# Optimization experiments

Measured on AMD Instinct MI355X. Metric: run time of the kernel, lower is better.

Reference implementation:

```python
import jax, jax.numpy as jnp
import numpy as np

EPS = 1e-5


def setup_inputs() -> dict:
    key = jax.random.key(0)
    ks = jax.random.split(key, 12)
    B, S, M, D, H, dh = 8, 512, 512, 1024, 16, 64
    T = S + M
    w_scale = 0.03  # keep attention logits in a sane range (mimics nn.Linear init scale)
    return {
        "x": jax.random.normal(ks[0], (B, S, D), jnp.float32),
        "mem": jax.random.normal(ks[1], (B, M, D), jnp.float32),
        "R": jax.random.normal(ks[2], (T, D), jnp.float32),
        "u": jax.random.normal(ks[3], (1, H, 1, dh), jnp.float32) * 0.1,
        "t": jax.random.normal(ks[4], (1, H, 1, dh), jnp.float32) * 0.1,
        "Wq": jax.random.normal(ks[5], (H * dh, D), jnp.float32) * w_scale,
        "Wk": jax.random.normal(ks[6], (H * dh, D), jnp.float32) * w_scale,
        "Wv": jax.random.normal(ks[7], (H * dh, D), jnp.float32) * w_scale,
        "Wr": jax.random.normal(ks[8], (H * dh, D), jnp.float32) * w_scale,
        "Wo": jax.random.normal(ks[9], (D, H * dh), jnp.float32) * w_scale,
        "gamma": jnp.ones((D,), jnp.float32),
        "beta": jnp.zeros((D,), jnp.float32),
    }


def reference(x, mem, R, u, t, Wq, Wk, Wv, Wr, Wo, gamma, beta):
    B, S, D = x.shape
    H, dh = u.shape[1], u.shape[3]
    h = jnp.concatenate([mem, x], axis=1)          # [B, T, D]
    T = h.shape[1]
    M = T - S

    q = (x @ Wq.T).reshape(B, S, H, dh).transpose(0, 2, 1, 3)   # [B,H,S,dh]
    k = (h @ Wk.T).reshape(B, T, H, dh).transpose(0, 2, 1, 3)   # [B,H,T,dh]
    v = (h @ Wv.T).reshape(B, T, H, dh).transpose(0, 2, 1, 3)   # [B,H,T,dh]
    r = (R[-T:] @ Wr.T).reshape(1, T, H, dh).transpose(0, 2, 1, 3)  # [1,H,T,dh]

    ac = jnp.einsum("bhid,bhjd->bhij", q + u, k)                # [B,H,S,T]
    bd = jnp.einsum("bhid,hjd->bhij", q + t, r[0])              # [B,H,S,T]

    # circulant shift: shifted[..., i, j] = bd[..., i, (j - i + S - 1) % T]
    idx = (jnp.arange(T)[None, :] - jnp.arange(S)[:, None] + S - 1) % T  # [S,T]
    bd = jnp.take_along_axis(bd, idx[None, None], axis=3)

    # causal mask with memory offset: keep j <= i + M (tril(mem_len)), then
    # exact-zero entries (the masked ones) become -inf, matching the original.
    mask = jnp.arange(T)[None, :] <= (jnp.arange(S)[:, None] + M)        # [S,T]
    score = jnp.where(mask[None, None], (ac + bd) / jnp.sqrt(jnp.float32(dh)), 0.0)
    score = jnp.where(score == 0, -jnp.inf, score)
    p = jax.nn.softmax(score, axis=-1)                                   # [B,H,S,T]

    att = jnp.einsum("bhij,bhjd->bhid", p, v).transpose(0, 2, 1, 3).reshape(B, S, H * dh)
    out = att @ Wo.T                                                      # dropout is identity (p=0/eval)

    y = out + x
    mu = jnp.mean(y, axis=-1, keepdims=True)
    var = jnp.var(y, axis=-1, keepdims=True)
    return (y - mu) / jnp.sqrt(var + EPS) * gamma + beta
```

## Files before the change

### kernel.cpp

```cpp
#include <hip/hip_runtime.h>
#include <math.h>

#define BB 8
#define SS 512
#define MM 512
#define TT 1024
#define DD 1024
#define HH 16
#define DH 64

typedef __attribute__((ext_vector_type(8))) short bf16x8;
typedef __attribute__((ext_vector_type(4))) float f32x4;

#define SCL2E 0.1803368801111f
#define DTHR 11.5f

__device__ __forceinline__ ushort f2bf(float f) {
  union { float f; unsigned u; } x; x.f = f;
  unsigned r = x.u + 0x7fffu + ((x.u >> 16) & 1u);
  return (ushort)(r >> 16);
}

__device__ __forceinline__ void stage16(void* lds, const void* g) {
  __builtin_amdgcn_global_load_lds((const __attribute__((address_space(1))) void*)g,
                                   (__attribute__((address_space(3))) void*)lds, 16, 0, 0);
}

template <int C>
__device__ __forceinline__ float dppf(float x) {
  return __builtin_bit_cast(float,
      __builtin_amdgcn_update_dpp(0, __builtin_bit_cast(int, x), C, 0xF, 0xF, true));
}
__device__ __forceinline__ float redmax16(float x) {
  x = fmaxf(x, dppf<0xB1>(x));
  x = fmaxf(x, dppf<0x4E>(x));
  x = fmaxf(x, dppf<0x141>(x));
  x = fmaxf(x, dppf<0x140>(x));
  return x;
}
__device__ __forceinline__ float redsum16(float x) {
  x += dppf<0xB1>(x);
  x += dppf<0x4E>(x);
  x += dppf<0x141>(x);
  x += dppf<0x140>(x);
  return x;
}
__device__ __forceinline__ float bperm_f(int byteaddr, float v) {
  return __builtin_bit_cast(float,
      __builtin_amdgcn_ds_bpermute(byteaddr, __builtin_bit_cast(int, v)));
}

__global__ __launch_bounds__(256) void cast_all(
    const float* __restrict__ mem, const float* __restrict__ x,
    const float* __restrict__ R, const float* __restrict__ Wq,
    const float* __restrict__ Wk, const float* __restrict__ Wv,
    const float* __restrict__ Wr, const float* __restrict__ Wo,
    ushort* __restrict__ hb, ushort* __restrict__ Rb, ushort* __restrict__ Wqb,
    ushort* __restrict__ Wkb, ushort* __restrict__ Wvb, ushort* __restrict__ Wrb,
    ushort* __restrict__ Wob) {
  const int M1 = 1 << 20;
  int i = (blockIdx.x * 256 + threadIdx.x) * 8;
  const float* src;
  ushort* dst;
  if (i < 4 * M1) {
    src = mem + i;
    dst = hb + (size_t)i + (size_t)(i >> 19) * 524288;
  } else if (i < 8 * M1) {
    int j = i - 4 * M1;
    src = x + j;
    dst = hb + (size_t)j + (size_t)(j >> 19) * 524288 + 524288;
  } else if (i < 9 * M1) {
    src = R + (i - 8 * M1);  dst = Rb + (i - 8 * M1);
  } else if (i < 10 * M1) {
    src = Wq + (i - 9 * M1); dst = Wqb + (i - 9 * M1);
  } else if (i < 11 * M1) {
    src = Wk + (i - 10 * M1); dst = Wkb + (i - 10 * M1);
  } else if (i < 12 * M1) {
    src = Wv + (i - 11 * M1); dst = Wvb + (i - 11 * M1);
  } else if (i < 13 * M1) {
    src = Wr + (i - 12 * M1); dst = Wrb + (i - 12 * M1);
  } else {
    src = Wo + (i - 13 * M1); dst = Wob + (i - 13 * M1);
  }
  float4 a = *(const float4*)(src);
  float4 c = *(const float4*)(src + 4);
  union { bf16x8 v; ushort u[8]; } pk;
  pk.u[0] = f2bf(a.x); pk.u[1] = f2bf(a.y); pk.u[2] = f2bf(a.z); pk.u[3] = f2bf(a.w);
  pk.u[4] = f2bf(c.x); pk.u[5] = f2bf(c.y); pk.u[6] = f2bf(c.z); pk.u[7] = f2bf(c.w);
  *(bf16x8*)(void*)dst = pk.v;
}

__global__ __launch_bounds__(256) void gemm_qkvr(
    const ushort* __restrict__ hb, const ushort* __restrict__ Rbuf,
    const ushort* __restrict__ Wqb, const ushort* __restrict__ Wkb,
    const ushort* __restrict__ Wvb, const ushort* __restrict__ Wrb,
    ushort* __restrict__ qub, ushort* __restrict__ qtb,
    ushort* __restrict__ kbo, ushort* __restrict__ vtb, ushort* __restrict__ rbo,
    const float* __restrict__ uvec, const float* __restrict__ tvec) {
  __shared__ ushort As[128 * 32];
  __shared__ ushort Bs[128 * 32];
  const int bid = blockIdx.x;
  const ushort* A;
  const ushort* W;
  ushort* C0 = nullptr;
  ushort* C1 = nullptr;
  bool dual = false, qslice = false, vmode = false;
  int mt, nx;
  if (bid < 256) {
    int r = bid; mt = r >> 3; nx = r & 7;
    A = hb; W = Wqb; C0 = qub; C1 = qtb; dual = true; qslice = true;
  } else if (bid < 768) {
    int r = bid - 256; mt = r >> 3; nx = r & 7;
    A = hb; W = Wkb; C0 = kbo;
  } else if (bid < 1280) {
    int r = bid - 768; mt = r >> 3; nx = r & 7;
    A = hb; W = Wvb; C0 = vtb; vmode = true;
  } else {
    int r = bid - 1280; mt = r >> 3; nx = r & 7;
    A = Rbuf; W = Wrb; C0 = rbo;
  }
  const int m0 = mt * 128, n0 = nx * 128;

  const int t = threadIdx.x;
  const int w = t >> 6, l = t & 63;
  const int m16 = l & 15, kg = l >> 4;
  const int wr = w >> 1, wc = w & 1;

  const int c0 = t, c1 = t + 256;
  const ushort* asrc0;
  const ushort* asrc1;
  {
    int gm0 = m0 + (c0 >> 2), gm1 = m0 + (c1 >> 2);
    if (qslice) {
      asrc0 = A + ((size_t)((gm0 >> 9) * TT + MM + (gm0 & 511))) * DD + (c0 & 3) * 8;
      asrc1 = A + ((size_t)((gm1 >> 9) * TT + MM + (gm1 & 511))) * DD + (c1 & 3) * 8;
    } else {
      asrc0 = A + (size_t)gm0 * DD + (c0 & 3) * 8;
      asrc1 = A + (size_t)gm1 * DD + (c1 & 3) * 8;
    }
  }
  const ushort* bsrc0 = W + (size_t)(n0 + (c0 >> 2)) * DD + (c0 & 3) * 8;
  const ushort* bsrc1 = W + (size_t)(n0 + (c1 >> 2)) * DD + (c1 & 3) * 8;
  ushort* adst0 = As + c0 * 8;
  ushort* adst1 = As + c1 * 8;
  ushort* bdst0 = Bs + c0 * 8;
  ushort* bdst1 = Bs + c1 * 8;

  f32x4 acc[4][4];
#pragma unroll
  for (int mi = 0; mi < 4; ++mi)
#pragma unroll
    for (int ni = 0; ni < 4; ++ni) acc[mi][ni] = (f32x4){0.f, 0.f, 0.f, 0.f};

  for (int k0 = 0; k0 < DD; k0 += 32) {
    stage16(adst0, asrc0 + k0);
    stage16(adst1, asrc1 + k0);
    stage16(bdst0, bsrc0 + k0);
    stage16(bdst1, bsrc1 + k0);
    __syncthreads();
    bf16x8 af[4], bfr[4];
#pragma unroll
    for (int mi = 0; mi < 4; ++mi)
      af[mi] = *(const bf16x8*)(const void*)&As[(wr * 64 + mi * 16 + m16) * 32 + kg * 8];
#pragma unroll
    for (int ni = 0; ni < 4; ++ni)
      bfr[ni] = *(const bf16x8*)(const void*)&Bs[(wc * 64 + ni * 16 + m16) * 32 + kg * 8];
#pragma unroll
    for (int mi = 0; mi < 4; ++mi)
#pragma unroll
      for (int ni = 0; ni < 4; ++ni)
        acc[mi][ni] = __builtin_amdgcn_mfma_f32_16x16x32_bf16(af[mi], bfr[ni], acc[mi][ni], 0, 0, 0);
    __syncthreads();
  }

  const int rbase = m0 + wr * 64 + kg * 4;
  const int cbase = n0 + wc * 64 + m16;
  if (vmode) {
    const int bb = m0 >> 10;
    const int tt0 = (m0 & 1023) + wr * 64 + kg * 4;
#pragma unroll
    for (int mi = 0; mi < 4; ++mi)
#pragma unroll
      for (int ni = 0; ni < 4; ++ni) {
        ushort4 o;
        o.x = f2bf(acc[mi][ni][0]); o.y = f2bf(acc[mi][ni][1]);
        o.z = f2bf(acc[mi][ni][2]); o.w = f2bf(acc[mi][ni][3]);
        *(ushort4*)(C0 + ((size_t)(bb * 1024 + cbase + ni * 16) << 10) + tt0 + mi * 16) = o;
      }
  } else if (dual) {
    float uv[4], tv[4];
#pragma unroll
    for (int ni = 0; ni < 4; ++ni) { uv[ni] = uvec[cbase + ni * 16]; tv[ni] = tvec[cbase + ni * 16]; }
#pragma unroll
    for (int mi = 0; mi < 4; ++mi)
#pragma unroll
      for (int ni = 0; ni < 4; ++ni)
#pragma unroll
        for (int rg = 0; rg < 4; ++rg) {
          size_t idx = (size_t)(rbase + mi * 16 + rg) * DD + cbase + ni * 16;
          C0[idx] = f2bf(acc[mi][ni][rg] + uv[ni]);
          C1[idx] = f2bf(acc[mi][ni][rg] + tv[ni]);
        }
  } else {
#pragma unroll
    for (int mi = 0; mi < 4; ++mi)
#pragma unroll
      for (int ni = 0; ni < 4; ++ni)
#pragma unroll
        for (int rg = 0; rg < 4; ++rg)
          C0[(size_t)(rbase + mi * 16 + rg) * DD + cbase + ni * 16] = f2bf(acc[mi][ni][rg]);
  }
}

__global__ __launch_bounds__(256) void gemm_wo(const ushort* __restrict__ A,
                                               const ushort* __restrict__ W,
                                               float* __restrict__ Cf) {
  __shared__ ushort As[128 * 32];
  __shared__ ushort Bs[128 * 32];
  const int t = threadIdx.x;
  const int w = t >> 6, l = t & 63;
  const int m16 = l & 15, kg = l >> 4;
  const int m0 = blockIdx.y * 128, n0 = blockIdx.x * 128;
  const int wr = w >> 1, wc = w & 1;

  const int c0 = t, c1 = t + 256;
  const ushort* asrc0 = A + (size_t)(m0 + (c0 >> 2)) * DD + (c0 & 3) * 8;
  const ushort* asrc1 = A + (size_t)(m0 + (c1 >> 2)) * DD + (c1 & 3) * 8;
  const ushort* bsrc0 = W + (size_t)(n0 + (c0 >> 2)) * DD + (c0 & 3) * 8;
  const ushort* bsrc1 = W + (size_t)(n0 + (c1 >> 2)) * DD + (c1 & 3) * 8;
  ushort* adst0 = As + c0 * 8;
  ushort* adst1 = As + c1 * 8;
  ushort* bdst0 = Bs + c0 * 8;
  ushort* bdst1 = Bs + c1 * 8;

  f32x4 acc[4][4];
#pragma unroll
  for (int mi = 0; mi < 4; ++mi)
#pragma unroll
    for (int ni = 0; ni < 4; ++ni) acc[mi][ni] = (f32x4){0.f, 0.f, 0.f, 0.f};

  for (int k0 = 0; k0 < DD; k0 += 32) {
    stage16(adst0, asrc0 + k0);
    stage16(adst1, asrc1 + k0);
    stage16(bdst0, bsrc0 + k0);
    stage16(bdst1, bsrc1 + k0);
    __syncthreads();
    bf16x8 af[4], bfr[4];
#pragma unroll
    for (int mi = 0; mi < 4; ++mi)
      af[mi] = *(const bf16x8*)(const void*)&As[(wr * 64 + mi * 16 + m16) * 32 + kg * 8];
#pragma unroll
    for (int ni = 0; ni < 4; ++ni)
      bfr[ni] = *(const bf16x8*)(const void*)&Bs[(wc * 64 + ni * 16 + m16) * 32 + kg * 8];
#pragma unroll
    for (int mi = 0; mi < 4; ++mi)
#pragma unroll
      for (int ni = 0; ni < 4; ++ni)
        acc[mi][ni] = __builtin_amdgcn_mfma_f32_16x16x32_bf16(af[mi], bfr[ni], acc[mi][ni], 0, 0, 0);
    __syncthreads();
  }

  const int rbase = m0 + wr * 64 + kg * 4;
  const int cbase = n0 + wc * 64 + m16;
#pragma unroll
  for (int mi = 0; mi < 4; ++mi)
#pragma unroll
    for (int ni = 0; ni < 4; ++ni)
#pragma unroll
      for (int rg = 0; rg < 4; ++rg)
        Cf[(size_t)(rbase + mi * 16 + rg) * DD + cbase + ni * 16] = acc[mi][ni][rg];
}

__global__ __launch_bounds__(256) void attn_mfma(const ushort* __restrict__ qu,
                                                 const ushort* __restrict__ qt,
                                                 const ushort* __restrict__ kb,
                                                 const ushort* __restrict__ vt,
                                                 const ushort* __restrict__ rb,
                                                 ushort* __restrict__ att) {
  const int w = threadIdx.x >> 6;
  const int l = threadIdx.x & 63;
  const int m16 = l & 15;
  const int kg = l >> 4;
  const int bid = blockIdx.x;
  const int it = 7 - (bid >> 7);
  const int bh = bid & 127;
  const int b = bh >> 4, h = bh & 15;
  const int i0 = it * 64;

  __shared__ ushort Ks[2][4096];
  __shared__ ushort Vs[4096];
  __shared__ ushort Rl[8192];
  __shared__ ushort plds[4][16][72];

  bf16x8 aqu[2], aqt[2];
  {
    const ushort* qrow = qu + ((size_t)(b * SS + i0 + w * 16 + m16)) * DD + h * DH + kg * 8;
    aqu[0] = *(const bf16x8*)(const void*)(qrow);
    aqu[1] = *(const bf16x8*)(const void*)(qrow + 32);
    const ushort* qrow2 = qt + ((size_t)(b * SS + i0 + w * 16 + m16)) * DD + h * DH + kg * 8;
    aqt[0] = *(const bf16x8*)(const void*)(qrow2);
    aqt[1] = *(const bf16x8*)(const void*)(qrow2 + 32);
  }

  int baddr[4];
  bool bsel[4];
#pragma unroll
  for (int rg = 0; rg < 4; ++rg) {
    const int rw = kg * 4 + rg;
    baddr[rg] = (kg * 16 + ((m16 + 15 - rw) & 15)) << 2;
    bsel[rg] = m16 > rw;
  }

  const int c0 = threadIdx.x, c1 = threadIdx.x + 256;
  const int r0 = c0 >> 3, sc0 = ((c0 & 7) * 8) ^ ((r0 & 7) << 3);
  const int r1 = c1 >> 3, sc1 = ((c1 & 7) * 8) ^ ((r1 & 7) << 3);
  const ushort* kp0 = kb + ((size_t)(b * TT) + r0) * DD + h * DH + sc0;
  const ushort* kp1 = kb + ((size_t)(b * TT) + r1) * DD + h * DH + sc1;
  const ushort* vp0 = vt + ((size_t)(b * 1024 + h * DH + r0)) * 1024 + sc0;
  const ushort* vp1 = vt + ((size_t)(b * 1024 + h * DH + r1)) * 1024 + sc1;

  const int cb0 = (kg * 8) ^ ((m16 & 7) << 3);
  const int cb1 = (kg * 8 + 32) ^ ((m16 & 7) << 3);
  int slot64[5];
#pragma unroll
  for (int f = 0; f < 5; ++f)
    slot64[f] = ((496 - i0 - w * 16 + m16 + f * 16) & 127) << 6;

  {
    const int base0 = 448 - i0;
#pragma unroll
    for (int kk = 0; kk < 4; ++kk) {
      int c = threadIdx.x + kk * 256;
      int ro = c >> 3, cc = c & 7;
      int p = base0 + ro;
      int slot = p & 127;
      stage16(Rl + slot * 64 + cc * 8,
              rb + (size_t)p * DD + h * DH + ((cc * 8) ^ ((ro & 7) << 3)));
    }
  }
  stage16(&Ks[0][c0 * 8], kp0);
  stage16(&Ks[0][c1 * 8], kp1);
  stage16(Vs + c0 * 8, vp0);
  stage16(Vs + c1 * 8, vp1);
  kp0 += (size_t)64 * DD; kp1 += (size_t)64 * DD;
  vp0 += 64; vp1 += 64;

  f32x4 O[4];
  float mrow[4], lrow[4];
#pragma unroll
  for (int nt = 0; nt < 4; ++nt) O[nt] = (f32x4){0.f, 0.f, 0.f, 0.f};
#pragma unroll
  for (int rg = 0; rg < 4; ++rg) { mrow[rg] = -1e30f; lrow[rg] = 0.f; }

  const int ntj = it + 9;
  int cur = 0;
  for (int jt = 0; jt < ntj; ++jt) {
    const int j0 = jt * 64;

    if (jt > 0) {
      stage16(Vs + c0 * 8, vp0);
      stage16(Vs + c1 * 8, vp1);
      vp0 += 64; vp1 += 64;
      const int pstart = 512 + j0 - i0;
#pragma unroll
      for (int kk = 0; kk < 2; ++kk) {
        int c = threadIdx.x + kk * 256;
        int ro = c >> 3, cc = c & 7;
        int p = pstart + ro;
        int pc = p < 1023 ? p : 1023;
        int slot = p & 127;
        stage16(Rl + slot * 64 + cc * 8,
                rb + (size_t)pc * DD + h * DH + ((cc * 8) ^ ((ro & 7) << 3)));
      }
    }
    __syncthreads();

    const ushort* kbase = &Ks[cur][0];
    f32x4 ac[4];
#pragma unroll
    for (int nt = 0; nt < 4; ++nt) {
      ac[nt] = (f32x4){0.f, 0.f, 0.f, 0.f};
      const int row = nt * 16 + m16;
#pragma unroll
      for (int ks = 0; ks < 2; ++ks) {
        bf16x8 bk = *(const bf16x8*)(const void*)(kbase + row * 64 + (ks == 0 ? cb0 : cb1));
        ac[nt] = __builtin_amdgcn_mfma_f32_16x16x32_bf16(aqu[ks], bk, ac[nt], 0, 0, 0);
      }
    }

    if (jt + 1 < ntj) {
      stage16(&Ks[cur ^ 1][c0 * 8], kp0);
      stage16(&Ks[cur ^ 1][c1 * 8], kp1);
      kp0 += (size_t)64 * DD; kp1 += (size_t)64 * DD;
    }

    f32x4 bd[5];
#pragma unroll
    for (int f = 0; f < 5; ++f) {
      f32x4 z = (f32x4){0.f, 0.f, 0.f, 0.f};
      bf16x8 b0 = *(const bf16x8*)(const void*)(Rl + slot64[f] + cb0);
      z = __builtin_amdgcn_mfma_f32_16x16x32_bf16(aqt[0], b0, z, 0, 0, 0);
      bf16x8 b1 = *(const bf16x8*)(const void*)(Rl + slot64[f] + cb1);
      bd[f] = __builtin_amdgcn_mfma_f32_16x16x32_bf16(aqt[1], b1, z, 0, 0, 0);
    }
#pragma unroll
    for (int f = 0; f < 5; ++f) slot64[f] = (slot64[f] + 4096) & 8191;

    float sca[4][4];
#pragma unroll
    for (int rg = 0; rg < 4; ++rg) {
      float rr[5];
#pragma unroll
      for (int f = 0; f < 5; ++f) rr[f] = bperm_f(baddr[rg], bd[f][rg]);
#pragma unroll
      for (int nt = 0; nt < 4; ++nt) {
        float bdv = bsel[rg] ? rr[nt + 1] : rr[nt];
        sca[nt][rg] = (ac[nt][rg] + bdv) * SCL2E;
      }
    }
    if (jt == ntj - 1) {
#pragma unroll
      for (int rg = 0; rg < 4; ++rg) {
        const int jmax = i0 + w * 16 + kg * 4 + rg + MM;
#pragma unroll
        for (int nt = 0; nt < 4; ++nt)
          sca[nt][rg] = (j0 + nt * 16 + m16 <= jmax) ? sca[nt][rg] : -1e30f;
      }
    }

    float pmax[4];
#pragma unroll
    for (int rg = 0; rg < 4; ++rg) {
      float pm = fmaxf(fmaxf(sca[0][rg], sca[1][rg]), fmaxf(sca[2][rg], sca[3][rg]));
      pmax[rg] = redmax16(pm);
    }
    bool grow = false;
#pragma unroll
    for (int rg = 0; rg < 4; ++rg) grow = grow || (pmax[rg] > mrow[rg] + DTHR);
    if (__any(grow)) {
#pragma unroll
      for (int rg = 0; rg < 4; ++rg) {
        float mnew = fmaxf(mrow[rg], pmax[rg]);
        float scale = __builtin_amdgcn_exp2f(mrow[rg] - mnew);
        mrow[rg] = mnew;
        lrow[rg] *= scale;
#pragma unroll
        for (int nt = 0; nt < 4; ++nt) O[nt][rg] *= scale;
      }
    }

#pragma unroll
    for (int rg = 0; rg < 4; ++rg) {
      float ps = 0.f;
#pragma unroll
      for (int nt = 0; nt < 4; ++nt) {
        float p = __builtin_amdgcn_exp2f(sca[nt][rg] - mrow[rg]);
        ps += p;
        plds[w][kg * 4 + rg][nt * 16 + m16] = f2bf(p);
      }
      lrow[rg] += redsum16(ps);
    }

#pragma unroll
    for (int ks = 0; ks < 2; ++ks) {
      bf16x8 pa = *(const bf16x8*)(const void*)&plds[w][m16][kg * 8 + ks * 32];
#pragma unroll
      for (int nt = 0; nt < 4; ++nt) {
        bf16x8 vf = *(const bf16x8*)(const void*)(Vs + (nt * 16 + m16) * 64 + (ks == 0 ? cb0 : cb1));
        O[nt] = __builtin_amdgcn_mfma_f32_16x16x32_bf16(pa, vf, O[nt], 0, 0, 0);
      }
    }

    __syncthreads();
    cur ^= 1;
  }

  float linv[4];
#pragma unroll
  for (int rg = 0; rg < 4; ++rg) linv[rg] = 1.f / lrow[rg];
#pragma unroll
  for (int nt = 0; nt < 4; ++nt) {
#pragma unroll
    for (int rg = 0; rg < 4; ++rg) {
      att[((size_t)(b * SS + i0 + w * 16 + kg * 4 + rg)) * DD + h * DH + nt * 16 + m16] =
          f2bf(O[nt][rg] * linv[rg]);
    }
  }
}

__global__ __launch_bounds__(256) void ln_kernel(const float* __restrict__ ypre,
                                                 const float* __restrict__ x,
                                                 const float* __restrict__ gamma,
                                                 const float* __restrict__ beta,
                                                 float* __restrict__ out) {
  const int row = blockIdx.x;
  const int t = threadIdx.x;
  const int lane = t & 63, w = t >> 6;
  const float* yr = ypre + (size_t)row * DD;
  const float* xr = x + (size_t)row * DD;

  float4 yv = *(const float4*)(yr + t * 4);
  float4 xv = *(const float4*)(xr + t * 4);
  float v0 = yv.x + xv.x, v1 = yv.y + xv.y, v2 = yv.z + xv.z, v3 = yv.w + xv.w;

  float s = v0 + v1 + v2 + v3;
  float ss = v0 * v0 + v1 * v1 + v2 * v2 + v3 * v3;
  __shared__ float rs[4], rss[4];
#pragma unroll
  for (int off = 32; off; off >>= 1) {
    s += __shfl_xor(s, off);
    ss += __shfl_xor(ss, off);
  }
  if (!lane) { rs[w] = s; rss[w] = ss; }
  __syncthreads();
  s = rs[0] + rs[1] + rs[2] + rs[3];
  ss = rss[0] + rss[1] + rss[2] + rss[3];
  const float mu = s * (1.f / DD);
  const float var = ss * (1.f / DD) - mu * mu;
  const float rstd = rsqrtf(var + 1e-5f);

  float4 g = *(const float4*)(gamma + t * 4);
  float4 be = *(const float4*)(beta + t * 4);
  float4 o;
  o.x = (v0 - mu) * rstd * g.x + be.x;
  o.y = (v1 - mu) * rstd * g.y + be.y;
  o.z = (v2 - mu) * rstd * g.z + be.z;
  o.w = (v3 - mu) * rstd * g.w + be.w;
  *(float4*)(out + (size_t)row * DD + t * 4) = o;
}

extern "C" void kernel_launch(void* const* d_in, const int* in_sizes, int n_in,
                              void* d_out, int out_size, void* d_ws, size_t ws_size,
                              hipStream_t stream) {
  const float* x = (const float*)d_in[0];
  const float* mem = (const float*)d_in[1];
  const float* R = (const float*)d_in[2];
  const float* u = (const float*)d_in[3];
  const float* tv = (const float*)d_in[4];
  const float* Wq = (const float*)d_in[5];
  const float* Wk = (const float*)d_in[6];
  const float* Wv = (const float*)d_in[7];
  const float* Wr = (const float*)d_in[8];
  const float* Wo = (const float*)d_in[9];
  const float* gamma = (const float*)d_in[10];
  const float* beta = (const float*)d_in[11];
  float* out = (float*)d_out;

  ushort* hb = (ushort*)d_ws;
  ushort* Rb = hb + (8u << 20);
  ushort* Wqb = Rb + (1u << 20);
  ushort* Wkb = Wqb + (1u << 20);
  ushort* Wvb = Wkb + (1u << 20);
  ushort* Wrb = Wvb + (1u << 20);
  ushort* Wob = Wrb + (1u << 20);
  ushort* qu_b = Wob + (1u << 20);
  ushort* qt_b = qu_b + (4u << 20);
  ushort* kb = qt_b + (4u << 20);
  ushort* vt = kb + (8u << 20);
  ushort* rb = vt + (8u << 20);
  ushort* att = qu_b;
  float* ypre = (float*)kb;

  dim3 blk(256);

  cast_all<<<dim3(7168), blk, 0, stream>>>(mem, x, R, Wq, Wk, Wv, Wr, Wo,
                                           hb, Rb, Wqb, Wkb, Wvb, Wrb, Wob);

  gemm_qkvr<<<dim3(1344), blk, 0, stream>>>(hb, Rb, Wqb, Wkb, Wvb, Wrb,
                                            qu_b, qt_b, kb, vt, rb, u, tv);

  attn_mfma<<<dim3(BB * HH * 8), blk, 0, stream>>>(qu_b, qt_b, kb, vt, rb, att);

  gemm_wo<<<dim3(8, 32), blk, 0, stream>>>(att, Wob, ypre);

  ln_kernel<<<dim3(BB * SS), blk, 0, stream>>>(ypre, x, gamma, beta, out);
}
```

Baseline: 195.2 us.

## Double-buffer LDS in projection GEMMs, remap blocks, and store Wo output as bf16

Both GEMM kernels now use two LDS buffers, so loads for the next K tile are issued before the MFMAs on the current tile. This replaces two __syncthreads per iteration with one waitcnt plus barrier. Block indices are remapped (XCD-style swizzle) to change which tiles run together, aiming at better L2 reuse. The Wo GEMM output is stored as bf16 instead of fp32 to halve the traffic into layernorm, which adds rounding error before the residual add.

```diff
diff --git a/kernel.cpp b/kernel.cpp
--- a/kernel.cpp
+++ b/kernel.cpp
@@ -19,6 +19,9 @@
   union { float f; unsigned u; } x; x.f = f;
   unsigned r = x.u + 0x7fffu + ((x.u >> 16) & 1u);
   return (ushort)(r >> 16);
+}
+__device__ __forceinline__ float bf2f(ushort u) {
+  return __builtin_bit_cast(float, ((unsigned)u) << 16);
 }
 
 __device__ __forceinline__ void stage16(void* lds, const void* g) {
@@ -97,9 +100,9 @@
     ushort* __restrict__ qub, ushort* __restrict__ qtb,
     ushort* __restrict__ kbo, ushort* __restrict__ vtb, ushort* __restrict__ rbo,
     const float* __restrict__ uvec, const float* __restrict__ tvec) {
-  __shared__ ushort As[128 * 32];
-  __shared__ ushort Bs[128 * 32];
-  const int bid = blockIdx.x;
+  __shared__ ushort As[2][4096];
+  __shared__ ushort Bs[2][4096];
+  const int bid = (blockIdx.x & 7) * 168 + (blockIdx.x >> 3);
   const ushort* A;
   const ushort* W;
   ushort* C0 = nullptr;
@@ -141,10 +144,6 @@
   }
   const ushort* bsrc0 = W + (size_t)(n0 + (c0 >> 2)) * DD + (c0 & 3) * 8;
   const ushort* bsrc1 = W + (size_t)(n0 + (c1 >> 2)) * DD + (c1 & 3) * 8;
-  ushort* adst0 = As + c0 * 8;
-  ushort* adst1 = As + c1 * 8;
-  ushort* bdst0 = Bs + c0 * 8;
-  ushort* bdst1 = Bs + c1 * 8;
 
   f32x4 acc[4][4];
 #pragma unroll
@@ -152,25 +151,39 @@
 #pragma unroll
     for (int ni = 0; ni < 4; ++ni) acc[mi][ni] = (f32x4){0.f, 0.f, 0.f, 0.f};
 
-  for (int k0 = 0; k0 < DD; k0 += 32) {
-    stage16(adst0, asrc0 + k0);
-    stage16(adst1, asrc1 + k0);
-    stage16(bdst0, bsrc0 + k0);
-    stage16(bdst1, bsrc1 + k0);
-    __syncthreads();
+  stage16(&As[0][c0 * 8], asrc0);
+  stage16(&As[0][c1 * 8], asrc1);
+  stage16(&Bs[0][c0 * 8], bsrc0);
+  stage16(&Bs[0][c1 * 8], bsrc1);
+  asm volatile("s_waitcnt vmcnt(0)" ::: "memory");
+  __builtin_amdgcn_s_barrier();
+
+#pragma unroll 2
+  for (int kt = 0; kt < 32; ++kt) {
+    const int bf = kt & 1;
+    if (kt < 31) {
+      const int k1 = (kt + 1) << 5;
+      stage16(&As[bf ^ 1][c0 * 8], asrc0 + k1);
+      stage16(&As[bf ^ 1][c1 * 8], asrc1 + k1);
+      stage16(&Bs[bf ^ 1][c0 * 8], bsrc0 + k1);
+      stage16(&Bs[bf ^ 1][c1 * 8], bsrc1 + k1);
+    }
     bf16x8 af[4], bfr[4];
 #pragma unroll
     for (int mi = 0; mi < 4; ++mi)
-      af[mi] = *(const bf16x8*)(const void*)&As[(wr * 64 + mi * 16 + m16) * 32 + kg * 8];
+      af[mi] = *(const bf16x8*)(const void*)&As[bf][(wr * 64 + mi * 16 + m16) * 32 + kg * 8];
 #pragma unroll
     for (int ni = 0; ni < 4; ++ni)
-      bfr[ni] = *(const bf16x8*)(const void*)&Bs[(wc * 64 + ni * 16 + m16) * 32 + kg * 8];
+      bfr[ni] = *(const bf16x8*)(const void*)&Bs[bf][(wc * 64 + ni * 16 + m16) * 32 + kg * 8];
 #pragma unroll
     for (int mi = 0; mi < 4; ++mi)
 #pragma unroll
       for (int ni = 0; ni < 4; ++ni)
         acc[mi][ni] = __builtin_amdgcn_mfma_f32_16x16x32_bf16(af[mi], bfr[ni], acc[mi][ni], 0, 0, 0);
-    __syncthreads();
+    if (kt < 31) {
+      asm volatile("s_waitcnt vmcnt(0)" ::: "memory");
+      __builtin_amdgcn_s_barrier();
+    }
   }
 
   const int rbase = m0 + wr * 64 + kg * 4;
@@ -214,13 +227,15 @@
 
 __global__ __launch_bounds__(256) void gemm_wo(const ushort* __restrict__ A,
                                                const ushort* __restrict__ W,
-                                               float* __restrict__ Cf) {
-  __shared__ ushort As[128 * 32];
-  __shared__ ushort Bs[128 * 32];
+                                               ushort* __restrict__ Cb) {
+  __shared__ ushort As[2][4096];
+  __shared__ ushort Bs[2][4096];
+  const int bid = (blockIdx.x & 7) * 32 + (blockIdx.x >> 3);
+  const int mt = bid >> 3, nx = bid & 7;
+  const int m0 = mt * 128, n0 = nx * 128;
   const int t = threadIdx.x;
   const int w = t >> 6, l = t & 63;
   const int m16 = l & 15, kg = l >> 4;
-  const int m0 = blockIdx.y * 128, n0 = blockIdx.x * 128;
   const int wr = w >> 1, wc = w & 1;
 
   const int c0 = t, c1 = t + 256;
@@ -228,10 +243,6 @@
   const ushort* asrc1 = A + (size_t)(m0 + (c1 >> 2)) * DD + (c1 & 3) * 8;
   const ushort* bsrc0 = W + (size_t)(n0 + (c0 >> 2)) * DD + (c0 & 3) * 8;
   const ushort* bsrc1 = W + (size_t)(n0 + (c1 >> 2)) * DD + (c1 & 3) * 8;
-  ushort* adst0 = As + c0 * 8;
-  ushort* adst1 = As + c1 * 8;
-  ushort* bdst0 = Bs + c0 * 8;
-  ushort* bdst1 = Bs + c1 * 8;
 
   f32x4 acc[4][4];
 #pragma unroll
@@ -239,25 +250,39 @@
 #pragma unroll
     for (int ni = 0; ni < 4; ++ni) acc[mi][ni] = (f32x4){0.f, 0.f, 0.f, 0.f};
 
-  for (int k0 = 0; k0 < DD; k0 += 32) {
-    stage16(adst0, asrc0 + k0);
-    stage16(adst1, asrc1 + k0);
-    stage16(bdst0, bsrc0 + k0);
-    stage16(bdst1, bsrc1 + k0);
-    __syncthreads();
+  stage16(&As[0][c0 * 8], asrc0);
+  stage16(&As[0][c1 * 8], asrc1);
+  stage16(&Bs[0][c0 * 8], bsrc0);
+  stage16(&Bs[0][c1 * 8], bsrc1);
+  asm volatile("s_waitcnt vmcnt(0)" ::: "memory");
+  __builtin_amdgcn_s_barrier();
+
+#pragma unroll 2
+  for (int kt = 0; kt < 32; ++kt) {
+    const int bf = kt & 1;
+    if (kt < 31) {
+      const int k1 = (kt + 1) << 5;
+      stage16(&As[bf ^ 1][c0 * 8], asrc0 + k1);
+      stage16(&As[bf ^ 1][c1 * 8], asrc1 + k1);
+      stage16(&Bs[bf ^ 1][c0 * 8], bsrc0 + k1);
+      stage16(&Bs[bf ^ 1][c1 * 8], bsrc1 + k1);
+    }
     bf16x8 af[4], bfr[4];
 #pragma unroll
     for (int mi = 0; mi < 4; ++mi)
-      af[mi] = *(const bf16x8*)(const void*)&As[(wr * 64 + mi * 16 + m16) * 32 + kg * 8];
+      af[mi] = *(const bf16x8*)(const void*)&As[bf][(wr * 64 + mi * 16 + m16) * 32 + kg * 8];
 #pragma unroll
     for (int ni = 0; ni < 4; ++ni)
-      bfr[ni] = *(const bf16x8*)(const void*)&Bs[(wc * 64 + ni * 16 + m16) * 32 + kg * 8];
+      bfr[ni] = *(const bf16x8*)(const void*)&Bs[bf][(wc * 64 + ni * 16 + m16) * 32 + kg * 8];
 #pragma unroll
     for (int mi = 0; mi < 4; ++mi)
 #pragma unroll
       for (int ni = 0; ni < 4; ++ni)
         acc[mi][ni] = __builtin_amdgcn_mfma_f32_16x16x32_bf16(af[mi], bfr[ni], acc[mi][ni], 0, 0, 0);
-    __syncthreads();
+    if (kt < 31) {
+      asm volatile("s_waitcnt vmcnt(0)" ::: "memory");
+      __builtin_amdgcn_s_barrier();
+    }
   }
 
   const int rbase = m0 + wr * 64 + kg * 4;
@@ -268,7 +293,7 @@
     for (int ni = 0; ni < 4; ++ni)
 #pragma unroll
       for (int rg = 0; rg < 4; ++rg)
-        Cf[(size_t)(rbase + mi * 16 + rg) * DD + cbase + ni * 16] = acc[mi][ni][rg];
+        Cb[(size_t)(rbase + mi * 16 + rg) * DD + cbase + ni * 16] = f2bf(acc[mi][ni][rg]);
 }
 
 __global__ __launch_bounds__(256) void attn_mfma(const ushort* __restrict__ qu,
@@ -488,7 +513,7 @@
   }
 }
 
-__global__ __launch_bounds__(256) void ln_kernel(const float* __restrict__ ypre,
+__global__ __launch_bounds__(256) void ln_kernel(const ushort* __restrict__ ypre,
                                                  const float* __restrict__ x,
                                                  const float* __restrict__ gamma,
                                                  const float* __restrict__ beta,
@@ -496,12 +521,13 @@
   const int row = blockIdx.x;
   const int t = threadIdx.x;
   const int lane = t & 63, w = t >> 6;
-  const float* yr = ypre + (size_t)row * DD;
+  const ushort* yr = ypre + (size_t)row * DD;
   const float* xr = x + (size_t)row * DD;
 
-  float4 yv = *(const float4*)(yr + t * 4);
+  ushort4 yv = *(const ushort4*)(yr + t * 4);
   float4 xv = *(const float4*)(xr + t * 4);
-  float v0 = yv.x + xv.x, v1 = yv.y + xv.y, v2 = yv.z + xv.z, v3 = yv.w + xv.w;
+  float v0 = bf2f(yv.x) + xv.x, v1 = bf2f(yv.y) + xv.y;
+  float v2 = bf2f(yv.z) + xv.z, v3 = bf2f(yv.w) + xv.w;
 
   float s = v0 + v1 + v2 + v3;
   float ss = v0 * v0 + v1 * v1 + v2 * v2 + v3 * v3;
@@ -559,7 +585,7 @@
   ushort* vt = kb + (8u << 20);
   ushort* rb = vt + (8u << 20);
   ushort* att = qu_b;
-  float* ypre = (float*)kb;
+  ushort* ypre = kb;
 
   dim3 blk(256);
 
@@ -571,7 +597,7 @@
 
   attn_mfma<<<dim3(BB * HH * 8), blk, 0, stream>>>(qu_b, qt_b, kb, vt, rb, att);
 
-  gemm_wo<<<dim3(8, 32), blk, 0, stream>>>(att, Wob, ypre);
+  gemm_wo<<<dim3(256), blk, 0, stream>>>(att, Wob, ypre);
 
   ln_kernel<<<dim3(BB * SS), blk, 0, stream>>>(ypre, x, gamma, beta, out);
 }
```

New measurement: 244.9 us. 25.5% more time.
